# Optimization experiments

Measured on AMD Instinct MI355X. Metric: run time of the kernel, lower is better.

Reference implementation:

```python
import jax, jax.numpy as jnp
import numpy as np

B, DIM, N_SIDE = 32, 256, 32
HEADS, DIM_K, DIM_U = 4, 16, 1
DIM_V = 64  # dim_out // heads
EPS = 1e-5

def _rel_pos_idx(n):
    # matches calc_rel_pos: meshgrid(ij) -> (N,2), pairwise diff + (n-1)
    i = np.arange(n)
    pos = np.stack(np.meshgrid(i, i, indexing='ij'), 0).reshape(2, -1).T  # (N, 2)
    rel = pos[None, :] - pos[:, None] + (n - 1)                            # (N, N, 2)
    return rel[..., 0], rel[..., 1]

def _bn(t, gamma, beta):
    # BatchNorm2d in training mode: batch stats over (B, H, W), biased var
    mu = t.mean(axis=(0, 2, 3), keepdims=True)
    var = t.var(axis=(0, 2, 3), keepdims=True)
    xhat = (t - mu) * jax.lax.rsqrt(var + EPS)
    return xhat * gamma[None, :, None, None] + beta[None, :, None, None]

def setup_inputs() -> dict:
    key = jax.random.key(0)
    ks = jax.random.split(key, 5)
    rl = 2 * N_SIDE - 1
    return {
        'x': jax.random.normal(ks[0], (B, DIM, N_SIDE, N_SIDE), jnp.float32),
        'w_q': jax.random.normal(ks[1], (DIM_K * HEADS, DIM), jnp.float32) * 0.05,
        'w_k': jax.random.normal(ks[2], (DIM_K * DIM_U, DIM), jnp.float32) * 0.05,
        'w_v': jax.random.normal(ks[3], (DIM_V * DIM_U, DIM), jnp.float32) * 0.05,
        'gamma_q': jnp.ones((DIM_K * HEADS,), jnp.float32),
        'beta_q': jnp.zeros((DIM_K * HEADS,), jnp.float32),
        'gamma_v': jnp.ones((DIM_V * DIM_U,), jnp.float32),
        'beta_v': jnp.zeros((DIM_V * DIM_U,), jnp.float32),
        'rel_pos_emb': jax.random.normal(ks[4], (rl, rl, DIM_K, DIM_U), jnp.float32),
    }

def reference(x, w_q, w_k, w_v, gamma_q, beta_q, gamma_v, beta_v, rel_pos_emb):
    b, c, hh, ww = x.shape
    n = hh * ww
    # 1x1 convs as channel contractions
    q = _bn(jnp.einsum('oc,bchw->bohw', w_q, x), gamma_q, beta_q)
    k = jnp.einsum('oc,bchw->bohw', w_k, x)
    v = _bn(jnp.einsum('oc,bchw->bohw', w_v, x), gamma_v, beta_v)
    q = q.reshape(b, HEADS, DIM_K, n)   # b h k n
    k = k.reshape(b, DIM_U, DIM_K, n)   # b u k m
    v = v.reshape(b, DIM_U, DIM_V, n)   # b u v m
    k = jax.nn.softmax(k, axis=-1)
    # content lambda
    lam_c = jnp.einsum('bukm,buvm->bkv', k, v)
    Yc = jnp.einsum('bhkn,bkv->bhvn', q, lam_c)
    # positional lambda via relative-position embedding gather
    ni, mi = _rel_pos_idx(N_SIDE)
    emb = rel_pos_emb[ni, mi]                      # (n, n, k, u)
    lam_p = jnp.einsum('nmku,buvm->bnkv', emb, v)  # dominant compute
    Yp = jnp.einsum('bhkn,bnkv->bhvn', q, lam_p)
    Y = Yc + Yp                                    # b h v n
    return Y.reshape(b, HEADS * DIM_V, hh, ww)
```

## Files before the change

kernel.cpp:

```cpp
#include <hip/hip_runtime.h>

using u16 = unsigned short;
using u32 = unsigned int;

typedef __attribute__((ext_vector_type(4))) float f32x4;
typedef __attribute__((ext_vector_type(4))) u16 u16x4;
typedef __attribute__((ext_vector_type(8))) u16 u16x8;
typedef __attribute__((ext_vector_type(8))) short s16x8;

__device__ __forceinline__ u16 f2bf(float f) {
  u32 x = __builtin_bit_cast(u32, f);
  x += 0x7fffu + ((x >> 16) & 1u);
  return (u16)(x >> 16);
}
__device__ __forceinline__ float bf2f(u16 u) {
  u32 x = ((u32)u) << 16;
  return __builtin_bit_cast(float, x);
}

__device__ __forceinline__ void glds16(const u16* gsrc, u16* ldst) {
  __builtin_amdgcn_global_load_lds(
      (const __attribute__((address_space(1))) unsigned int*)gsrc,
      (__attribute__((address_space(3))) unsigned int*)ldst, 16, 0, 0);
}

__global__ __launch_bounds__(256) void k_prep(
    const float* __restrict__ wq, const float* __restrict__ wk,
    const float* __restrict__ wv, const float* __restrict__ R,
    u16* __restrict__ Wb, u16* __restrict__ APre)
{
  const int blk = blockIdx.x;
  const int t = threadIdx.x;
  if (blk < 144) {
    const int o = blk;
    const float* src = (o < 64) ? (wq + o * 256)
                     : (o < 80) ? (wk + (o - 64) * 256)
                                : (wv + (o - 80) * 256);
    Wb[o * 256 + t] = f2bf(src[t]);
  } else {
    const int di = blk - 144;
    const int w = t >> 6, l = t & 63;
    const int g = l >> 4, k = l & 15;
    for (int j1 = w; j1 < 32; j1 += 4) {
      u16x8 o8;
#pragma unroll
      for (int e = 0; e < 8; ++e) {
        int dj = 8 * g + e - j1 + 31;
        o8[e] = f2bf(R[(di * 63 + dj) * 16 + k]);
      }
      *(u16x8*)(APre + ((di * 32 + j1) * 64 + l) * 8) = o8;
    }
  }
}

__global__ __launch_bounds__(256) void k_proj(
    const float* __restrict__ x, const u16* __restrict__ Wb,
    float* __restrict__ q_raw, float* __restrict__ k_raw,
    float* __restrict__ v_raw)
{
  __shared__ u16 XLb[64][264];
  const int b  = blockIdx.x >> 4;
  const int p0 = (blockIdx.x & 15) * 64;
  const int t  = threadIdx.x;

  {
    const int p4 = (t & 15) * 4;
    const int cb = (t >> 4);
#pragma unroll
    for (int i = 0; i < 8; ++i) {
      const int c = 2 * (i * 16 + cb);
      f32x4 xa = *(const f32x4*)&x[(b * 256 + c) * 1024 + p0 + p4];
      f32x4 xb = *(const f32x4*)&x[(b * 256 + c + 1) * 1024 + p0 + p4];
#pragma unroll
      for (int j = 0; j < 4; ++j) {
        u32 pk = (u32)f2bf(xa[j]) | ((u32)f2bf(xb[j]) << 16);
        *(u32*)&XLb[p4 + j][c] = pk;
      }
    }
  }
  __syncthreads();

  const int w  = t >> 6;
  const int l  = t & 63;
  const int g  = l >> 4;
  const int cc = l & 15;
  const int p  = p0 + w * 16 + cc;

  f32x4 acc[9];
  const f32x4 fz = {0.f, 0.f, 0.f, 0.f};
#pragma unroll
  for (int mt = 0; mt < 9; ++mt) acc[mt] = fz;

#pragma unroll
  for (int ko = 0; ko < 8; ++ko) {
    s16x8 bfr = *(const s16x8*)&XLb[w * 16 + cc][ko * 32 + g * 8];
#pragma unroll
    for (int mt = 0; mt < 9; ++mt) {
      s16x8 afr = *(const s16x8*)&Wb[(mt * 16 + cc) * 256 + ko * 32 + g * 8];
      acc[mt] = __builtin_amdgcn_mfma_f32_16x16x32_bf16(afr, bfr, acc[mt], 0, 0, 0);
    }
  }

#pragma unroll
  for (int mt = 0; mt < 9; ++mt) {
#pragma unroll
    for (int r = 0; r < 4; ++r) {
      const int o = mt * 16 + 4 * g + r;
      const float val = acc[mt][r];
      if (mt < 4)       q_raw[(b * 64 + o) * 1024 + p] = val;
      else if (mt == 4) k_raw[(b * 16 + (o - 64)) * 1024 + p] = val;
      else              v_raw[(b * 64 + (o - 80)) * 1024 + p] = val;
    }
  }
}

__global__ __launch_bounds__(256) void k_stats(
    const float* __restrict__ q_raw, const float* __restrict__ v_raw,
    const float* __restrict__ k_raw,
    float* __restrict__ qs1, float* __restrict__ qs2,
    float* __restrict__ vs1, float* __restrict__ vs2,
    float* __restrict__ kmax, float* __restrict__ kinv)
{
  const int blk = blockIdx.x;
  const int t = threadIdx.x;
  const int w = t >> 6, lane = t & 63;
  if (blk < 128) {
    const float* src = (blk < 64) ? q_raw : v_raw;
    float* s1g = (blk < 64) ? qs1 : vs1;
    float* s2g = (blk < 64) ? qs2 : vs2;
    const int rv0 = (blk & 63) * 32;
    for (int rr = w; rr < 32; rr += 4) {
      const int rv = rv0 + rr;
      const float* row = src + rv * 1024;
      float s1 = 0.f, s2 = 0.f;
      for (int m = lane; m < 1024; m += 64) { float xx = row[m]; s1 += xx; s2 += xx * xx; }
#pragma unroll
      for (int off = 32; off; off >>= 1) { s1 += __shfl_down(s1, off); s2 += __shfl_down(s2, off); }
      if (lane == 0) { atomicAdd(&s1g[rv & 63], s1); atomicAdd(&s2g[rv & 63], s2); }
    }
  } else {
    const int j = blk - 128;
    for (int rr = w * 2; rr < w * 2 + 2; ++rr) {
      const int row = j * 8 + rr;
      const float* kr = k_raw + row * 1024;
      float mx = -3.0e38f;
      for (int m = lane; m < 1024; m += 64) mx = fmaxf(mx, kr[m]);
#pragma unroll
      for (int off = 32; off; off >>= 1) mx = fmaxf(mx, __shfl_xor(mx, off));
      float s = 0.f;
      for (int m = lane; m < 1024; m += 64) s += __expf(kr[m] - mx);
#pragma unroll
      for (int off = 32; off; off >>= 1) s += __shfl_xor(s, off);
      if (lane == 0) { kmax[row] = mx; kinv[row] = 1.0f / s; }
    }
  }
}

__global__ __launch_bounds__(256) void k_norm(
    const float* __restrict__ v_raw,
    const float* __restrict__ vs1, const float* __restrict__ vs2,
    const float* __restrict__ gv, const float* __restrict__ bv,
    u16* __restrict__ vn, u16* __restrict__ vnF)
{
  const int b  = blockIdx.x >> 5;
  const int i2 = blockIdx.x & 31;
  const int t  = threadIdx.x;
  const int tt = t >> 6, l = t & 63;
  const int v  = tt * 16 + (l & 15);
  const int m8 = i2 * 32 + (l >> 4) * 8;
  const float invN = 1.0f / 32768.0f;
  const float mu = vs1[v] * invN;
  const float var = vs2[v] * invN - mu * mu;
  const float rs = rsqrtf(var + 1e-5f);
  const float sc = rs * gv[v];
  const float bi = bv[v] - mu * sc;
  const float* src = v_raw + (b * 64 + v) * 1024 + m8;
  f32x4 a = *(const f32x4*)src;
  f32x4 c = *(const f32x4*)(src + 4);
  u16x8 o8;
#pragma unroll
  for (int j = 0; j < 4; ++j) o8[j] = f2bf(a[j] * sc + bi);
#pragma unroll
  for (int j = 0; j < 4; ++j) o8[4 + j] = f2bf(c[j] * sc + bi);
  *(u16x8*)&vnF[((b * 32 + i2) * 4 + tt) * 512 + l * 8] = o8;
  *(u16x8*)&vn[(b * 64 + v) * 1024 + m8] = o8;
}

__global__ __launch_bounds__(256) void k_lamc(
    const float* __restrict__ k_raw, const float* __restrict__ kmax,
    const float* __restrict__ kinv, const u16* __restrict__ vn,
    float* __restrict__ lam_c)
{
  __shared__ float KE[16][132];
  const int b  = blockIdx.x >> 3;
  const int m0 = (blockIdx.x & 7) * 128;
  const int t  = threadIdx.x;
  {
    const int kc = t >> 4, mm = (t & 15) * 8;
    const int row = b * 16 + kc;
    const float* kr = k_raw + row * 1024 + m0 + mm;
    const float mx = kmax[row], iv = kinv[row];
#pragma unroll
    for (int j = 0; j < 8; ++j) KE[kc][mm + j] = __expf(kr[j] - mx) * iv;
  }
  __syncthreads();
  const int kc = t & 15, vg = t >> 4;
  const u16* vb = vn + b * 65536 + m0;
  float acc[4] = {0.f, 0.f, 0.f, 0.f};
  for (int m4 = 0; m4 < 128; m4 += 4) {
    f32x4 ke = *(const f32x4*)&KE[kc][m4];
#pragma unroll
    for (int j = 0; j < 4; ++j) {
      u16x4 vv = *(const u16x4*)&vb[(vg * 4 + j) * 1024 + m4];
      acc[j] += ke[0] * bf2f(vv[0]) + ke[1] * bf2f(vv[1])
              + ke[2] * bf2f(vv[2]) + ke[3] * bf2f(vv[3]);
    }
  }
#pragma unroll
  for (int j = 0; j < 4; ++j)
    atomicAdd(&lam_c[(b * 16 + kc) * 64 + vg * 4 + j], acc[j]);
}

__device__ __forceinline__ void load_a4(s16x8 (&dst)[4], const u16* ab)
{
#pragma unroll
  for (int j = 0; j < 4; ++j) dst[j] = *(const s16x8*)(ab + j * 512);
}

union KMainSmem {
  u16 BB[2][8192];
  float YL[256][18];
};

__global__ __launch_bounds__(256, 4) void k_main(
    const u16* __restrict__ APre, const u16* __restrict__ vnF,
    const float* __restrict__ q_raw, const float* __restrict__ lam_c,
    const float* __restrict__ qs1, const float* __restrict__ qs2,
    const float* __restrict__ gq, const float* __restrict__ bq,
    float* __restrict__ out)
{
  __shared__ alignas(16) KMainSmem S;
  __shared__ float QL[64][17];
  const int bid  = blockIdx.x;
  const int xcd  = bid & 7;
  const int sb   = bid >> 3;
  const int b    = xcd * 4 + (sb & 3);
  const int rest = sb >> 2;
  const int i1   = rest >> 1;
  const int half = rest & 1;
  const int t  = threadIdx.x;
  const int w  = t >> 6;
  const int l  = t & 63;
  const int g  = l >> 4;
  const int c  = l & 15;
  const int j1base = half * 16 + w * 4;

  const u16* vF = vnF + b * 65536;

  f32x4 acc[4][4];
  const f32x4 fz = {0.f, 0.f, 0.f, 0.f};
#pragma unroll
  for (int nn = 0; nn < 4; ++nn)
#pragma unroll
    for (int tt = 0; tt < 4; ++tt) acc[nn][tt] = fz;

  {
    const int o = t >> 2, ns = (t & 3) * 4;
    const float invN = 1.0f / 32768.0f;
    const float mu = qs1[o] * invN;
    const float var = qs2[o] * invN - mu * mu;
    const float rs = rsqrtf(var + 1e-5f);
    const float sc = rs * gq[o];
    const float bi = bq[o] - mu * sc;
    f32x4 qa = *(const f32x4*)&q_raw[(b * 64 + o) * 1024 + i1 * 32 + half * 16 + ns];
#pragma unroll
    for (int j = 0; j < 4; ++j) QL[o][ns + j] = qa[j] * sc + bi;
  }
  {
    const u16* src = vF + w * 2048 + l * 8;
    u16* dst = &S.BB[0][w * 2048];
#pragma unroll
    for (int j = 0; j < 4; ++j) glds16(src + j * 512, dst + j * 512);
  }

  s16x8 afrP[4], afrQ[4];
  const u16* aBase = APre + ((31 - i1) * 32 + j1base) * 512 + l * 8;
  load_a4(afrP, aBase);
  __syncthreads();

  for (int p = 0; p < 8; ++p) {
    const int cur = p & 1;
    const bool pf = (p < 7);
    if (pf) {
      const u16* src = vF + (p + 1) * 8192 + w * 2048 + l * 8;
      u16* dst = &S.BB[cur ^ 1][w * 2048];
#pragma unroll
      for (int j = 0; j < 4; ++j) glds16(src + j * 512, dst + j * 512);
    }
    __builtin_amdgcn_sched_barrier(0);
    const u16* ap = aBase + 4 * p * 16384;
    s16x8 bfr[4];
#pragma unroll
    for (int s = 0; s < 4; ++s) {
#pragma unroll
      for (int tt = 0; tt < 4; ++tt)
        bfr[tt] = *(const s16x8*)&S.BB[cur][s * 2048 + tt * 512 + l * 8];
      if (s < 3) {
        if (s & 1) load_a4(afrP, ap + (s + 1) * 16384);
        else       load_a4(afrQ, ap + (s + 1) * 16384);
      } else if (pf) {
        load_a4(afrP, ap + 4 * 16384);
      }
      const s16x8* A = (s & 1) ? afrQ : afrP;
#pragma unroll
      for (int nn = 0; nn < 4; ++nn)
#pragma unroll
        for (int tt = 0; tt < 4; ++tt)
          acc[nn][tt] = __builtin_amdgcn_mfma_f32_16x16x32_bf16(
              A[nn], bfr[tt], acc[nn][tt], 0, 0, 0);
    }
    asm volatile("s_waitcnt vmcnt(4)" ::: "memory");
    __builtin_amdgcn_sched_barrier(0);
    __builtin_amdgcn_s_barrier();
    __builtin_amdgcn_sched_barrier(0);
  }

  {
    const float* lcb = lam_c + b * 1024;
#pragma unroll
    for (int tt = 0; tt < 4; ++tt)
#pragma unroll
      for (int r = 0; r < 4; ++r) {
        const float lv = lcb[(4 * g + r) * 64 + tt * 16 + c];
#pragma unroll
        for (int nn = 0; nn < 4; ++nn) acc[nn][tt][r] += lv;
      }
  }
#pragma unroll
  for (int nn = 0; nn < 4; ++nn) {
    const int j1loc = w * 4 + nn;
#pragma unroll
    for (int h = 0; h < 4; ++h) {
      const float q0 = QL[h * 16 + 4 * g + 0][j1loc];
      const float q1 = QL[h * 16 + 4 * g + 1][j1loc];
      const float q2 = QL[h * 16 + 4 * g + 2][j1loc];
      const float q3 = QL[h * 16 + 4 * g + 3][j1loc];
#pragma unroll
      for (int tt = 0; tt < 4; ++tt) {
        float sY = q0 * acc[nn][tt][0] + q1 * acc[nn][tt][1]
                 + q2 * acc[nn][tt][2] + q3 * acc[nn][tt][3];
        sY += __shfl_xor(sY, 16);
        sY += __shfl_xor(sY, 32);
        if (g == h) S.YL[h * 64 + tt * 16 + c][j1loc] = sY;
      }
    }
  }
  __syncthreads();
#pragma unroll
  for (int it = 0; it < 4; ++it) {
    const int o  = (t >> 2) + it * 64;
    const int nf = (t & 3) * 4;
    f32x4 v4 = *(const f32x4*)&S.YL[o][nf];
    *(f32x4*)&out[(b * 256 + o) * 1024 + i1 * 32 + half * 16 + nf] = v4;
  }
}

extern "C" void kernel_launch(void* const* d_in, const int* in_sizes, int n_in,
                              void* d_out, int out_size, void* d_ws, size_t ws_size,
                              hipStream_t stream) {
  const float* x  = (const float*)d_in[0];
  const float* wq = (const float*)d_in[1];
  const float* wk = (const float*)d_in[2];
  const float* wv = (const float*)d_in[3];
  const float* gq = (const float*)d_in[4];
  const float* bq = (const float*)d_in[5];
  const float* gv = (const float*)d_in[6];
  const float* bv = (const float*)d_in[7];
  const float* R  = (const float*)d_in[8];
  float* out = (float*)d_out;

  float* wsf   = (float*)d_ws;
  float* q_raw = wsf;
  float* k_raw = q_raw + 32 * 64 * 1024;
  float* v_raw = k_raw + 32 * 16 * 1024;
  float* lam_c = v_raw + 32 * 64 * 1024;
  float* qs1   = lam_c + 32 * 16 * 64;
  float* qs2   = qs1 + 64;
  float* vs1   = qs2 + 64;
  float* vs2   = vs1 + 64;
  float* kmax  = vs2 + 64;
  float* kinv  = kmax + 512;
  u16*   vn    = (u16*)(kinv + 512);
  u16*   vnF   = vn + 32 * 64 * 1024;
  u16*   APre  = vnF + 32 * 65536;
  u16*   Wb    = APre + 63 * 32 * 512;

  hipMemsetAsync(lam_c, 0, (32 * 16 * 64 + 256) * sizeof(float), stream);
  k_prep<<<207, 256, 0, stream>>>(wq, wk, wv, R, Wb, APre);
  k_proj<<<512, 256, 0, stream>>>(x, Wb, q_raw, k_raw, v_raw);
  k_stats<<<192, 256, 0, stream>>>(q_raw, v_raw, k_raw, qs1, qs2, vs1, vs2, kmax, kinv);
  k_norm<<<1024, 256, 0, stream>>>(v_raw, vs1, vs2, gv, bv, vn, vnF);
  k_lamc<<<256, 256, 0, stream>>>(k_raw, kmax, kinv, vn, lam_c);
  k_main<<<2048, 256, 0, stream>>>(APre, vnF, q_raw, lam_c, qs1, qs2, gq, bq, out);
}
```

Before: 165.4 us.

## Fuse BN statistics into projection and merge V-normalization with content lambda

Batch-norm sum and sum-of-squares for q and v are now reduced inside the projection kernel from MFMA accumulators, first through shared memory and then with global atomics. This removes a separate pass that re-read q_raw and v_raw. The k softmax stats move into a small vectorized kernel. The V normalization is fused into the content-lambda kernel, which keeps normalized V in shared fp32, so the bf16 row-major vn buffer is no longer written or read. This drops one launch and several full-tensor memory passes, at the cost of more shared-memory atomics in k_proj and a larger shared footprint in the fused kernel.

Result: faster. 138.3 us (-16.4%).

```diff
diff --git a/kernel.cpp b/kernel.cpp
--- a/kernel.cpp
+++ b/kernel.cpp
@@ -53,12 +53,19 @@
   }
 }
 
+union ProjSmem {
+  u16 XLb[64][264];
+  float SS[2][160];
+};
+
 __global__ __launch_bounds__(256) void k_proj(
     const float* __restrict__ x, const u16* __restrict__ Wb,
     float* __restrict__ q_raw, float* __restrict__ k_raw,
-    float* __restrict__ v_raw)
-{
-  __shared__ u16 XLb[64][264];
+    float* __restrict__ v_raw,
+    float* __restrict__ qs1, float* __restrict__ qs2,
+    float* __restrict__ vs1, float* __restrict__ vs2)
+{
+  __shared__ ProjSmem PS;
   const int b  = blockIdx.x >> 4;
   const int p0 = (blockIdx.x & 15) * 64;
   const int t  = threadIdx.x;
@@ -74,7 +81,7 @@
 #pragma unroll
       for (int j = 0; j < 4; ++j) {
         u32 pk = (u32)f2bf(xa[j]) | ((u32)f2bf(xb[j]) << 16);
-        *(u32*)&XLb[p4 + j][c] = pk;
+        *(u32*)&PS.XLb[p4 + j][c] = pk;
       }
     }
   }
@@ -93,7 +100,7 @@
 
 #pragma unroll
   for (int ko = 0; ko < 8; ++ko) {
-    s16x8 bfr = *(const s16x8*)&XLb[w * 16 + cc][ko * 32 + g * 8];
+    s16x8 bfr = *(const s16x8*)&PS.XLb[w * 16 + cc][ko * 32 + g * 8];
 #pragma unroll
     for (int mt = 0; mt < 9; ++mt) {
       s16x8 afr = *(const s16x8*)&Wb[(mt * 16 + cc) * 256 + ko * 32 + g * 8];
@@ -112,90 +119,109 @@
       else              v_raw[(b * 64 + (o - 80)) * 1024 + p] = val;
     }
   }
-}
-
-__global__ __launch_bounds__(256) void k_stats(
-    const float* __restrict__ q_raw, const float* __restrict__ v_raw,
+
+  __syncthreads();
+  {
+    float* ss = &PS.SS[0][0];
+    for (int i = t; i < 320; i += 256) ss[i] = 0.f;
+  }
+  __syncthreads();
+#pragma unroll
+  for (int mt = 0; mt < 9; ++mt) {
+    if (mt == 4) continue;
+#pragma unroll
+    for (int r = 0; r < 4; ++r) {
+      float s1 = acc[mt][r];
+      float s2 = s1 * s1;
+#pragma unroll
+      for (int off = 1; off < 16; off <<= 1) {
+        s1 += __shfl_xor(s1, off);
+        s2 += __shfl_xor(s2, off);
+      }
+      if (cc == 0) {
+        const int o = mt * 16 + 4 * g + r;
+        atomicAdd(&PS.SS[0][o], s1);
+        atomicAdd(&PS.SS[1][o], s2);
+      }
+    }
+  }
+  __syncthreads();
+  if (t < 64) {
+    atomicAdd(&qs1[t], PS.SS[0][t]);
+    atomicAdd(&qs2[t], PS.SS[1][t]);
+  } else if (t >= 80 && t < 144) {
+    atomicAdd(&vs1[t - 80], PS.SS[0][t]);
+    atomicAdd(&vs2[t - 80], PS.SS[1][t]);
+  }
+}
+
+__global__ __launch_bounds__(256) void k_soft(
     const float* __restrict__ k_raw,
-    float* __restrict__ qs1, float* __restrict__ qs2,
-    float* __restrict__ vs1, float* __restrict__ vs2,
     float* __restrict__ kmax, float* __restrict__ kinv)
 {
-  const int blk = blockIdx.x;
   const int t = threadIdx.x;
   const int w = t >> 6, lane = t & 63;
-  if (blk < 128) {
-    const float* src = (blk < 64) ? q_raw : v_raw;
-    float* s1g = (blk < 64) ? qs1 : vs1;
-    float* s2g = (blk < 64) ? qs2 : vs2;
-    const int rv0 = (blk & 63) * 32;
-    for (int rr = w; rr < 32; rr += 4) {
-      const int rv = rv0 + rr;
-      const float* row = src + rv * 1024;
-      float s1 = 0.f, s2 = 0.f;
-      for (int m = lane; m < 1024; m += 64) { float xx = row[m]; s1 += xx; s2 += xx * xx; }
-#pragma unroll
-      for (int off = 32; off; off >>= 1) { s1 += __shfl_down(s1, off); s2 += __shfl_down(s2, off); }
-      if (lane == 0) { atomicAdd(&s1g[rv & 63], s1); atomicAdd(&s2g[rv & 63], s2); }
-    }
-  } else {
-    const int j = blk - 128;
-    for (int rr = w * 2; rr < w * 2 + 2; ++rr) {
-      const int row = j * 8 + rr;
-      const float* kr = k_raw + row * 1024;
-      float mx = -3.0e38f;
-      for (int m = lane; m < 1024; m += 64) mx = fmaxf(mx, kr[m]);
-#pragma unroll
-      for (int off = 32; off; off >>= 1) mx = fmaxf(mx, __shfl_xor(mx, off));
-      float s = 0.f;
-      for (int m = lane; m < 1024; m += 64) s += __expf(kr[m] - mx);
-#pragma unroll
-      for (int off = 32; off; off >>= 1) s += __shfl_xor(s, off);
-      if (lane == 0) { kmax[row] = mx; kinv[row] = 1.0f / s; }
-    }
-  }
-}
-
-__global__ __launch_bounds__(256) void k_norm(
+  const int row = blockIdx.x * 4 + w;
+  const f32x4* kr4 = (const f32x4*)(k_raw + row * 1024 + lane * 16);
+  f32x4 a0 = kr4[0], a1 = kr4[1], a2 = kr4[2], a3 = kr4[3];
+  float mx = -3.0e38f;
+#pragma unroll
+  for (int j = 0; j < 4; ++j)
+    mx = fmaxf(mx, fmaxf(fmaxf(a0[j], a1[j]), fmaxf(a2[j], a3[j])));
+#pragma unroll
+  for (int off = 32; off; off >>= 1) mx = fmaxf(mx, __shfl_xor(mx, off));
+  float s = 0.f;
+#pragma unroll
+  for (int j = 0; j < 4; ++j)
+    s += __expf(a0[j] - mx) + __expf(a1[j] - mx)
+       + __expf(a2[j] - mx) + __expf(a3[j] - mx);
+#pragma unroll
+  for (int off = 32; off; off >>= 1) s += __shfl_xor(s, off);
+  if (lane == 0) { kmax[row] = mx; kinv[row] = 1.0f / s; }
+}
+
+__global__ __launch_bounds__(256) void k_nl(
     const float* __restrict__ v_raw,
     const float* __restrict__ vs1, const float* __restrict__ vs2,
     const float* __restrict__ gv, const float* __restrict__ bv,
-    u16* __restrict__ vn, u16* __restrict__ vnF)
-{
-  const int b  = blockIdx.x >> 5;
-  const int i2 = blockIdx.x & 31;
-  const int t  = threadIdx.x;
-  const int tt = t >> 6, l = t & 63;
-  const int v  = tt * 16 + (l & 15);
-  const int m8 = i2 * 32 + (l >> 4) * 8;
-  const float invN = 1.0f / 32768.0f;
-  const float mu = vs1[v] * invN;
-  const float var = vs2[v] * invN - mu * mu;
-  const float rs = rsqrtf(var + 1e-5f);
-  const float sc = rs * gv[v];
-  const float bi = bv[v] - mu * sc;
-  const float* src = v_raw + (b * 64 + v) * 1024 + m8;
-  f32x4 a = *(const f32x4*)src;
-  f32x4 c = *(const f32x4*)(src + 4);
-  u16x8 o8;
-#pragma unroll
-  for (int j = 0; j < 4; ++j) o8[j] = f2bf(a[j] * sc + bi);
-#pragma unroll
-  for (int j = 0; j < 4; ++j) o8[4 + j] = f2bf(c[j] * sc + bi);
-  *(u16x8*)&vnF[((b * 32 + i2) * 4 + tt) * 512 + l * 8] = o8;
-  *(u16x8*)&vn[(b * 64 + v) * 1024 + m8] = o8;
-}
-
-__global__ __launch_bounds__(256) void k_lamc(
     const float* __restrict__ k_raw, const float* __restrict__ kmax,
-    const float* __restrict__ kinv, const u16* __restrict__ vn,
-    float* __restrict__ lam_c)
-{
+    const float* __restrict__ kinv,
+    u16* __restrict__ vnF, float* __restrict__ lam_c)
+{
+  __shared__ float VN[64][136];
   __shared__ float KE[16][132];
   const int b  = blockIdx.x >> 3;
   const int m0 = (blockIdx.x & 7) * 128;
   const int t  = threadIdx.x;
   {
+    const int v = t & 63, mseg = t >> 6;
+    const float invN = 1.0f / 32768.0f;
+    const float mu = vs1[v] * invN;
+    const float var = vs2[v] * invN - mu * mu;
+    const float sc = rsqrtf(var + 1e-5f) * gv[v];
+    const float bi = bv[v] - mu * sc;
+    const int i2 = (m0 >> 5) + mseg;
+    const float* src = v_raw + (b * 64 + v) * 1024 + i2 * 32;
+    u16* dstF = vnF + ((b * 32 + i2) * 4 + (v >> 4)) * 512 + (v & 15) * 8;
+#pragma unroll
+    for (int lg = 0; lg < 4; ++lg) {
+      f32x4 a = *(const f32x4*)(src + lg * 8);
+      f32x4 c = *(const f32x4*)(src + lg * 8 + 4);
+      f32x4 na, nc;
+      u16x8 o8;
+#pragma unroll
+      for (int j = 0; j < 4; ++j) {
+        na[j] = a[j] * sc + bi;
+        nc[j] = c[j] * sc + bi;
+        o8[j] = f2bf(na[j]);
+        o8[4 + j] = f2bf(nc[j]);
+      }
+      *(f32x4*)&VN[v][mseg * 32 + lg * 8] = na;
+      *(f32x4*)&VN[v][mseg * 32 + lg * 8 + 4] = nc;
+      *(u16x8*)(dstF + lg * 128) = o8;
+    }
+  }
+  {
     const int kc = t >> 4, mm = (t & 15) * 8;
     const int row = b * 16 + kc;
     const float* kr = k_raw + row * 1024 + m0 + mm;
@@ -205,15 +231,13 @@
   }
   __syncthreads();
   const int kc = t & 15, vg = t >> 4;
-  const u16* vb = vn + b * 65536 + m0;
   float acc[4] = {0.f, 0.f, 0.f, 0.f};
   for (int m4 = 0; m4 < 128; m4 += 4) {
     f32x4 ke = *(const f32x4*)&KE[kc][m4];
 #pragma unroll
     for (int j = 0; j < 4; ++j) {
-      u16x4 vv = *(const u16x4*)&vb[(vg * 4 + j) * 1024 + m4];
-      acc[j] += ke[0] * bf2f(vv[0]) + ke[1] * bf2f(vv[1])
-              + ke[2] * bf2f(vv[2]) + ke[3] * bf2f(vv[3]);
+      f32x4 vv = *(const f32x4*)&VN[vg * 4 + j][m4];
+      acc[j] += ke[0] * vv[0] + ke[1] * vv[1] + ke[2] * vv[2] + ke[3] * vv[3];
     }
   }
 #pragma unroll
@@ -397,9 +421,8 @@
 
   hipMemsetAsync(lam_c, 0, (32 * 16 * 64 + 256) * sizeof(float), stream);
   k_prep<<<207, 256, 0, stream>>>(wq, wk, wv, R, Wb, APre);
-  k_proj<<<512, 256, 0, stream>>>(x, Wb, q_raw, k_raw, v_raw);
-  k_stats<<<192, 256, 0, stream>>>(q_raw, v_raw, k_raw, qs1, qs2, vs1, vs2, kmax, kinv);
-  k_norm<<<1024, 256, 0, stream>>>(v_raw, vs1, vs2, gv, bv, vn, vnF);
-  k_lamc<<<256, 256, 0, stream>>>(k_raw, kmax, kinv, vn, lam_c);
+  k_proj<<<512, 256, 0, stream>>>(x, Wb, q_raw, k_raw, v_raw, qs1, qs2, vs1, vs2);
+  k_soft<<<128, 256, 0, stream>>>(k_raw, kmax, kinv);
+  k_nl<<<256, 256, 0, stream>>>(v_raw, vs1, vs2, gv, bv, k_raw, kmax, kinv, vnF, lam_c);
   k_main<<<2048, 256, 0, stream>>>(APre, vnF, q_raw, lam_c, qs1, qs2, gq, bq, out);
 }
```
